# Kernel tuning notes

Measured on AMD Instinct MI355X. Metric: run time of the kernel, lower is better.

The kernel has to match this reference:

```python
import jax, jax.numpy as jnp
import numpy as np

N, E = 25000, 400000
D_NODE, D_EDGE_IN, D_EH, D_H, D_DUAL = 128, 16, 128, 256, 128


def layer_norm(x, g, b, eps=1e-5):
    mu = jnp.mean(x, axis=-1, keepdims=True)
    var = jnp.mean((x - mu) ** 2, axis=-1, keepdims=True)
    return (x - mu) * jax.lax.rsqrt(var + eps) * g + b


def setup_inputs() -> dict:
    key = jax.random.key(0)
    ks = jax.random.split(key, 20)

    def w(k, shape):
        return (jax.random.normal(k, shape, dtype=jnp.float32) * 0.05)

    inp = {
        "node_embedding": jax.random.normal(ks[0], (N, D_NODE), dtype=jnp.float32),
        "edge_index": jax.random.randint(ks[1], (2, E), 0, N, dtype=jnp.int64),
        "edge_attr": jax.random.normal(ks[2], (E, D_EDGE_IN), dtype=jnp.float32),
        "dual_node_emb": jax.random.normal(ks[3], (E, D_DUAL), dtype=jnp.float32),
        "atom_reactivity_logits": jax.random.normal(ks[4], (N,), dtype=jnp.float32),
        "W_be1": w(ks[5], (D_EDGE_IN, D_EH)), "b_be1": jnp.zeros((D_EH,), jnp.float32),
        "g_be1": jnp.ones((D_EH,), jnp.float32), "bb_be1": jnp.zeros((D_EH,), jnp.float32),
        "W_be2": w(ks[6], (D_EH, D_EH)), "b_be2": jnp.zeros((D_EH,), jnp.float32),
        "g_be2": jnp.ones((D_EH,), jnp.float32), "bb_be2": jnp.zeros((D_EH,), jnp.float32),
        "W_be3": w(ks[7], (D_EH, D_EH)), "b_be3": jnp.zeros((D_EH,), jnp.float32),
        "g_be3": jnp.ones((D_EH,), jnp.float32), "bb_be3": jnp.zeros((D_EH,), jnp.float32),
        # DualGraphBondReactivityPredictor
        "W_d1": w(ks[8], (D_DUAL, D_H)), "b_d1": jnp.zeros((D_H,), jnp.float32),
        "W_d2": w(ks[9], (D_H, D_H)), "b_d2": jnp.zeros((D_H,), jnp.float32),
        "W_do": w(ks[10], (D_H, 1)), "b_do": jnp.zeros((1,), jnp.float32),
        # main head: in = 2*D_NODE + D_EH + 3 = 387
        "W_f1": w(ks[11], (2 * D_NODE + D_EH + 3, D_H)), "b_f1": jnp.zeros((D_H,), jnp.float32),
        "W_f2": w(ks[12], (D_H, D_H)), "b_f2": jnp.zeros((D_H,), jnp.float32),
        "W_bo": w(ks[13], (D_H, 1)), "b_bo": jnp.zeros((1,), jnp.float32),
    }
    return inp


def reference(node_embedding, edge_index, edge_attr, dual_node_emb, atom_reactivity_logits,
              W_be1, b_be1, g_be1, bb_be1, W_be2, b_be2, g_be2, bb_be2,
              W_be3, b_be3, g_be3, bb_be3,
              W_d1, b_d1, W_d2, b_d2, W_do, b_do,
              W_f1, b_f1, W_f2, b_f2, W_bo, b_bo):
    src, dst = edge_index[0], edge_index[1]

    # BondEmbedding (dropout = identity in eval mode)
    e = jax.nn.silu(layer_norm(edge_attr @ W_be1 + b_be1, g_be1, bb_be1))
    e = jax.nn.silu(layer_norm(e @ W_be2 + b_be2, g_be2, bb_be2))
    e = jax.nn.silu(layer_norm(e @ W_be3 + b_be3, g_be3, bb_be3))  # [E, D_EH]

    atom_p = jax.nn.sigmoid(atom_reactivity_logits)  # [N]
    p_src = atom_p[src][:, None]  # [E,1]
    p_dst = atom_p[dst][:, None]

    # dual-graph bond reactivity
    d = jax.nn.silu(dual_node_emb @ W_d1 + b_d1)
    d = jax.nn.silu(d @ W_d2 + b_d2)
    dual_p = jax.nn.sigmoid((d @ W_do + b_do)[:, 0])[:, None]  # [E,1]

    feats = jnp.concatenate(
        [node_embedding[src], node_embedding[dst], e, dual_p, p_src, p_dst], axis=-1
    )  # [E, 2*D_NODE + D_EH + 3]

    x = jax.nn.silu(feats @ W_f1 + b_f1)
    x = jax.nn.silu(x @ W_f2 + b_f2)
    return (x @ W_bo + b_bo)[:, 0]  # [E]
```

## Files before the change

### kernel.cpp

```cpp
#include <hip/hip_runtime.h>
#include <hip/hip_bf16.h>
#include <stdint.h>

typedef __attribute__((ext_vector_type(8))) short bf16x8;
typedef __attribute__((ext_vector_type(4))) float f32x4;
typedef __attribute__((ext_vector_type(4))) float float4v;

__device__ __forceinline__ uint16_t bfc(float x){
    __hip_bfloat16 h = __float2bfloat16(x);
    return __builtin_bit_cast(uint16_t, h);
}
__device__ __forceinline__ uint32_t pk2(float a, float b){
    return (uint32_t)bfc(a) | ((uint32_t)bfc(b) << 16);
}
__device__ __forceinline__ float fsigmoid(float x){ return 1.0f / (1.0f + __expf(-x)); }
__device__ __forceinline__ float fsilu(float x){ return x * fsigmoid(x); }

__device__ __forceinline__ bf16x8 pack8(float4v lo, float4v hi){
    bf16x8 r;
    r[0]=(short)bfc(lo[0]); r[1]=(short)bfc(lo[1]);
    r[2]=(short)bfc(lo[2]); r[3]=(short)bfc(lo[3]);
    r[4]=(short)bfc(hi[0]); r[5]=(short)bfc(hi[1]);
    r[6]=(short)bfc(hi[2]); r[7]=(short)bfc(hi[3]);
    return r;
}

#define SZ_BE1 4096
#define SZ_128 16384
#define SZ_D1  32768
#define SZ_D2  65536
#define SZ_F1  98304
#define OFF_BE1 0
#define OFF_BE2 (OFF_BE1 + SZ_BE1)
#define OFF_BE3 (OFF_BE2 + SZ_128)
#define OFF_D1  (OFF_BE3 + SZ_128)
#define OFF_D2  (OFF_D1 + SZ_D1)
#define OFF_F1  (OFF_D2 + SZ_D2)
#define OFF_F2  (OFF_F1 + SZ_F1)
#define WS_ELEMS (OFF_F2 + SZ_D2)

__device__ __forceinline__ int fragpos(int k, int c, int OUT){
    int kt = k >> 5, ct = c >> 4;
    int fid = kt * (OUT >> 4) + ct;
    int ln = ((k & 31) >> 3) * 16 + (c & 15);
    return fid * 512 + ln * 8 + (k & 7);
}

__global__ void __launch_bounds__(256)
prep_w(const float* __restrict__ Wbe1, const float* __restrict__ Wbe2,
       const float* __restrict__ Wbe3, const float* __restrict__ Wd1,
       const float* __restrict__ Wd2,  const float* __restrict__ Wf1,
       const float* __restrict__ Wf2,  uint16_t* __restrict__ ws){
    int t = blockIdx.x * 256 + threadIdx.x;
    if (t >= WS_ELEMS) return;
    if (t < OFF_BE2) {
        int u = t;            int k = u >> 7, c = u & 127;
        float v = (k < 16) ? Wbe1[k * 128 + c] : 0.0f;
        ws[OFF_BE1 + fragpos(k, c, 128)] = bfc(v);
    } else if (t < OFF_BE3) {
        int u = t - OFF_BE2;  int k = u >> 7, c = u & 127;
        ws[OFF_BE2 + fragpos(k, c, 128)] = bfc(Wbe2[u]);
    } else if (t < OFF_D1) {
        int u = t - OFF_BE3;  int k = u >> 7, c = u & 127;
        ws[OFF_BE3 + fragpos(k, c, 128)] = bfc(Wbe3[u]);
    } else if (t < OFF_D2) {
        int u = t - OFF_D1;   int k = u >> 8, c = u & 255;
        ws[OFF_D1 + fragpos(k, c, 256)] = bfc(Wd1[u]);
    } else if (t < OFF_F1) {
        int u = t - OFF_D2;   int k = u >> 8, c = u & 255;
        ws[OFF_D2 + fragpos(k, c, 256)] = bfc(Wd2[u]);
    } else if (t < OFF_F2) {
        int u = t - OFF_F1;   int k = u >> 8, c = u & 255;
        ws[OFF_F1 + fragpos(k, c, 256)] = bfc(Wf1[u]);
    } else {
        int u = t - OFF_F2;   int k = u >> 8, c = u & 255;
        ws[OFF_F2 + fragpos(k, c, 256)] = bfc(Wf2[u]);
    }
}

__global__ void __launch_bounds__(256)
prep_n(const float* __restrict__ src, uint16_t* __restrict__ dst, int n){
    int t = blockIdx.x * 256 + threadIdx.x;
    if (t < n) dst[t] = bfc(src[t]);
}

typedef const __attribute__((address_space(1))) void gas_void;
typedef __attribute__((address_space(3))) void las_void;
__device__ __forceinline__ void g2l16(const void* g, void* l){
    __builtin_amdgcn_global_load_lds((gas_void*)g, (las_void*)l, 16, 0, 0);
}


__global__ void __launch_bounds__(512)
k_be(const float* __restrict__ edge_attr,
     const float* __restrict__ b_be1, const float* __restrict__ g_be1, const float* __restrict__ bb_be1,
     const float* __restrict__ b_be2, const float* __restrict__ g_be2, const float* __restrict__ bb_be2,
     const float* __restrict__ b_be3, const float* __restrict__ g_be3, const float* __restrict__ bb_be3,
     const uint16_t* __restrict__ ws, uint16_t* __restrict__ e3buf, int E)
{
    __shared__ char lds[49152];
    const int t = threadIdx.x, wave = t >> 6, lane = t & 63;
    const int li = lane & 15, lg = lane >> 4;
    const int e0b = blockIdx.x * 128;
    char* bufE = lds;
    uint16_t* wb0 = (uint16_t*)(lds + 32768);
    uint16_t* wb1 = (uint16_t*)(lds + 40960);
    const uint8_t* wsb = (const uint8_t*)ws;

    int cur = 0;
// ... 55 lines not shown
            const float* pa = edge_attr + (size_t)ea * 16 + lg * 8;
            aE = pack8(*(const float4v*)pa, *(const float4v*)(pa + 4));
        }
        grpBE(aE);
        lnstoreBE(g_be1, bb_be1);
        stepend();
    }
    initBE(b_be2);
    #pragma unroll 1
    for (int kt = 0; kt < 4; ++kt){
        stage8(kt < 3 ? OFF_BE2 + (kt + 1) * 4096 : OFF_BE3);
        grpBE(eb_read(wave * 16 + li, kt));
        if (kt == 3) lnstoreBE(g_be2, bb_be2);
        stepend();
    }
    initBE(b_be3);
    #pragma unroll 1
    for (int kt = 0; kt < 4; ++kt){
        if (kt < 3) stage8(OFF_BE3 + (kt + 1) * 4096);
        grpBE(eb_read(wave * 16 + li, kt));
        if (kt == 3) lnstoreBE(g_be3, bb_be3);
        stepend();
    }
    #pragma unroll
    for (int i = 0; i < 4; ++i){
        int b = t * 16 + i * 8192;
        int row = b >> 8;
        uint4 v = *(const uint4*)(bufE + (b ^ ((row & 7) << 4)));
        *(uint4*)((uint8_t*)e3buf + (size_t)e0b * 256 + b) = v;
    }
}

__global__ void __launch_bounds__(512)
k_d1(const float* __restrict__ dual_emb, const float* __restrict__ b_d1,
     const uint16_t* __restrict__ ws, uint16_t* __restrict__ hbuf, int E)
{
    __shared__ char lds[32768];
    const int t = threadIdx.x, wave = t >> 6, lane = t & 63;
    const int li = lane & 15, lg = lane >> 4;
    const int eg = wave >> 1, ch = wave & 1;
    const int e0b = blockIdx.x * 128;
    uint16_t* wb0 = (uint16_t*)lds;
    uint16_t* wb1 = (uint16_t*)(lds + 16384);
    const uint8_t* wsb = (const uint8_t*)ws;

    int cur = 0;
    auto stage16 = [&](int elemoff){
        uint8_t* dst = (uint8_t*)(cur ? wb0 : wb1) + t * 16;
        const uint8_t* g = wsb + (size_t)elemoff * 2 + t * 16;
        g2l16(g, dst); g2l16(g + 8192, dst + 8192);
    };
    auto stepend = [&](){ __syncthreads(); cur ^= 1; };
    auto curb = [&]() -> const uint16_t* { return cur ? wb1 : wb0; };

    f32x4 acc[2][8];
    #pragma unroll
    for (int ct = 0; ct < 8; ++ct){
        float bv = b_d1[ch * 128 + ct * 16 + li];
        f32x4 iv = {bv, bv, bv, bv};
        acc[0][ct] = iv; acc[1][ct] = iv;
    }

    {
        const uint8_t* g = wsb + (size_t)OFF_D1 * 2 + t * 16;
        g2l16(g, (uint8_t*)wb0 + t * 16);
        g2l16(g + 8192, (uint8_t*)wb0 + t * 16 + 8192);
    }
    __syncthreads();

    #pragma unroll 1
    for (int kt = 0; kt < 4; ++kt){
        if (kt < 3) stage16(OFF_D1 + (kt + 1) * 8192);
        bf16x8 a0, a1;
        {
            int ea = e0b + eg * 32 + li;      if (ea >= E) ea = E - 1;
            int eb = e0b + eg * 32 + 16 + li; if (eb >= E) eb = E - 1;
            const float* pa = dual_emb + (size_t)ea * 128 + kt * 32 + lg * 8;
            const float* pb = dual_emb + (size_t)eb * 128 + kt * 32 + lg * 8;
            a0 = pack8(*(const float4v*)pa, *(const float4v*)(pa + 4));
            a1 = pack8(*(const float4v*)pb, *(const float4v*)(pb + 4));
        }
        #pragma unroll
        for (int ct = 0; ct < 8; ++ct){
            bf16x8 b = *(const bf16x8*)(curb() + (ch * 8 + ct) * 512 + lane * 8);
            acc[0][ct] = __builtin_amdgcn_mfma_f32_16x16x32_bf16(a0, b, acc[0][ct], 0, 0, 0);
            acc[1][ct] = __builtin_amdgcn_mfma_f32_16x16x32_bf16(a1, b, acc[1][ct], 0, 0, 0);
        }
        if (kt < 3) stepend();
    }
    #pragma unroll
    for (int rt = 0; rt < 2; ++rt)
        #pragma unroll
        for (int r = 0; r < 4; ++r){
            size_t row = (size_t)(e0b + eg * 32 + rt * 16 + lg * 4 + r);
            #pragma unroll
            for (int ct = 0; ct < 8; ++ct)
                hbuf[row * 256 + ch * 128 + ct * 16 + li] = bfc(fsilu(acc[rt][ct][r]));
        }
}

__global__ void __launch_bounds__(512)
k_d2(const float* __restrict__ b_d2, const float* __restrict__ W_do, const float* __restrict__ b_do,
     const uint16_t* __restrict__ ws, const uint16_t* __restrict__ hbuf,
     float* __restrict__ dpbuf, int E)
{
    __shared__ char lds[33792];
    const int t = threadIdx.x, wave = t >> 6, lane = t & 63;
    const int li = lane & 15, lg = lane >> 4;
    const int eg = wave >> 1, ch = wave & 1;
    const int e0b = blockIdx.x * 128;
    uint16_t* wb0 = (uint16_t*)lds;
    uint16_t* wb1 = (uint16_t*)(lds + 16384);
    float* dpp = (float*)(lds + 32768);
    const uint8_t* wsb = (const uint8_t*)ws;

    int cur = 0;
    auto stage16 = [&](int elemoff){
        uint8_t* dst = (uint8_t*)(cur ? wb0 : wb1) + t * 16;
        const uint8_t* g = wsb + (size_t)elemoff * 2 + t * 16;
        g2l16(g, dst); g2l16(g + 8192, dst + 8192);
    };
    auto stepend = [&](){ __syncthreads(); cur ^= 1; };
    auto curb = [&]() -> const uint16_t* { return cur ? wb1 : wb0; };

    f32x4 acc[2][8];
    #pragma unroll
    for (int ct = 0; ct < 8; ++ct){
        float bv = b_d2[ch * 128 + ct * 16 + li];
        f32x4 iv = {bv, bv, bv, bv};
        acc[0][ct] = iv; acc[1][ct] = iv;
    }
    {
        const uint8_t* g = wsb + (size_t)OFF_D2 * 2 + t * 16;
        g2l16(g, (uint8_t*)wb0 + t * 16);
        g2l16(g + 8192, (uint8_t*)wb0 + t * 16 + 8192);
    }
    __syncthreads();

    #pragma unroll 1
    for (int kt = 0; kt < 8; ++kt){
        if (kt < 7) stage16(OFF_D2 + (kt + 1) * 8192);
        bf16x8 a0 = *(const bf16x8*)(hbuf + (size_t)(e0b + eg * 32 + li) * 256 + kt * 32 + lg * 8);
        bf16x8 a1 = *(const bf16x8*)(hbuf + (size_t)(e0b + eg * 32 + 16 + li) * 256 + kt * 32 + lg * 8);
        #pragma unroll
        for (int ct = 0; ct < 8; ++ct){
            bf16x8 b = *(const bf16x8*)(curb() + (ch * 8 + ct) * 512 + lane * 8);
            acc[0][ct] = __builtin_amdgcn_mfma_f32_16x16x32_bf16(a0, b, acc[0][ct], 0, 0, 0);
            acc[1][ct] = __builtin_amdgcn_mfma_f32_16x16x32_bf16(a1, b, acc[1][ct], 0, 0, 0);
        }
        if (kt < 7) stepend();
    }
    #pragma unroll
    for (int rt = 0; rt < 2; ++rt)
        #pragma unroll
        for (int r = 0; r < 4; ++r){
            float s = 0.f;
            #pragma unroll
            for (int ct = 0; ct < 8; ++ct)
                s += fsilu(acc[rt][ct][r]) * W_do[ch * 128 + ct * 16 + li];
            s += __shfl_xor(s, 1); s += __shfl_xor(s, 2);
            s += __shfl_xor(s, 4); s += __shfl_xor(s, 8);
            if (li == 0) dpp[ch * 128 + eg * 32 + rt * 16 + lg * 4 + r] = s;
        }
    __syncthreads();
    if (t < 128) dpbuf[e0b + t] = fsigmoid(dpp[t] + dpp[128 + t] + b_do[0]);
}

__global__ void __launch_bounds__(512)
k_f1(const int* __restrict__ edge_index, const float* __restrict__ logits,
     const float* __restrict__ W_f1, const float* __restrict__ b_f1,
     const uint16_t* __restrict__ ws, const uint16_t* __restrict__ nbf,
     const uint16_t* __restrict__ e3buf, const float* __restrict__ dpbuf,
     uint16_t* __restrict__ hbuf, int E)
{
    __shared__ char lds[34816];
    const int t = threadIdx.x, wave = t >> 6, lane = t & 63;
    const int li = lane & 15, lg = lane >> 4;
    const int eg = wave >> 1, ch = wave & 1;
    const int e0b = blockIdx.x * 128;
    uint16_t* wb0 = (uint16_t*)lds;
    uint16_t* wb1 = (uint16_t*)(lds + 16384);
    float* ps = (float*)(lds + 32768);
    float* pd = (float*)(lds + 33280);
    int* sidx = (int*)(lds + 33792);
    int* didx = (int*)(lds + 34304);
    const uint8_t* wsb = (const uint8_t*)ws;

    if (t < 128) {
        int e = e0b + t; if (e >= E) e = E - 1;
        int s_ = edge_index[e];
        int d_ = edge_index[E + e];
        sidx[t] = s_; didx[t] = d_;
        ps[t] = fsigmoid(logits[s_]);
        pd[t] = fsigmoid(logits[d_]);
    }
    int cur = 0;
    auto stage16 = [&](int elemoff){
        uint8_t* dst = (uint8_t*)(cur ? wb0 : wb1) + t * 16;
        const uint8_t* g = wsb + (size_t)elemoff * 2 + t * 16;
        g2l16(g, dst); g2l16(g + 8192, dst + 8192);
    };
    auto stepend = [&](){ __syncthreads(); cur ^= 1; };
    auto curb = [&]() -> const uint16_t* { return cur ? wb1 : wb0; };

    {
        const uint8_t* g = wsb + (size_t)OFF_F1 * 2 + t * 16;
        g2l16(g, (uint8_t*)wb0 + t * 16);
        g2l16(g + 8192, (uint8_t*)wb0 + t * 16 + 8192);
    }
    __syncthreads();

    f32x4 acc[2][8];
    {
        #pragma unroll
        for (int ct = 0; ct < 8; ++ct){
            int col = ch * 128 + ct * 16 + li;
            float bv = b_f1[col];
            float t0 = W_f1[384 * 256 + col];
            float t1 = W_f1[385 * 256 + col];
            float t2 = W_f1[386 * 256 + col];
            #pragma unroll
            for (int rt = 0; rt < 2; ++rt)
                #pragma unroll
                for (int r = 0; r < 4; ++r){
                    int row = eg * 32 + rt * 16 + lg * 4 + r;
                    float dv = dpbuf[e0b + row];
                    acc[rt][ct][r] = bv + dv*t0 + ps[row]*t1 + pd[row]*t2;
                }
        }
    }
    int s0 = sidx[eg * 32 + li],  s1 = sidx[eg * 32 + 16 + li];
    int d0 = didx[eg * 32 + li],  d1 = didx[eg * 32 + 16 + li];
    #pragma unroll 1
    for (int kt = 0; kt < 12; ++kt){
        if (kt < 11) stage16(OFF_F1 + (kt + 1) * 8192);
        bf16x8 a0, a1;
        if (kt < 8){
            int ra = (kt < 4) ? s0 : d0;
            int rb = (kt < 4) ? s1 : d1;
            int ko = (kt & 3) * 32 + lg * 8;
            a0 = *(const bf16x8*)(nbf + (size_t)ra * 128 + ko);
            a1 = *(const bf16x8*)(nbf + (size_t)rb * 128 + ko);
        } else {
            int ko = (kt - 8) * 32 + lg * 8;
            a0 = *(const bf16x8*)(e3buf + (size_t)(e0b + eg * 32 + li) * 128 + ko);
            a1 = *(const bf16x8*)(e3buf + (size_t)(e0b + eg * 32 + 16 + li) * 128 + ko);
        }
        #pragma unroll
        for (int ct = 0; ct < 8; ++ct){
            bf16x8 b = *(const bf16x8*)(curb() + (ch * 8 + ct) * 512 + lane * 8);
            acc[0][ct] = __builtin_amdgcn_mfma_f32_16x16x32_bf16(a0, b, acc[0][ct], 0, 0, 0);
            acc[1][ct] = __builtin_amdgcn_mfma_f32_16x16x32_bf16(a1, b, acc[1][ct], 0, 0, 0);
        }
        if (kt < 11) stepend();
    }
    #pragma unroll
    for (int rt = 0; rt < 2; ++rt)
        #pragma unroll
        for (int r = 0; r < 4; ++r){
            size_t row = (size_t)(e0b + eg * 32 + rt * 16 + lg * 4 + r);
            #pragma unroll
            for (int ct = 0; ct < 8; ++ct)
                hbuf[row * 256 + ch * 128 + ct * 16 + li] = bfc(fsilu(acc[rt][ct][r]));
        }
}

__global__ void __launch_bounds__(512)
k_f2(const float* __restrict__ b_f2, const float* __restrict__ W_bo, const float* __restrict__ b_bo,
     const uint16_t* __restrict__ ws, const uint16_t* __restrict__ hbuf,
     float* __restrict__ out, int E)
{
    __shared__ char lds[33792];
    const int t = threadIdx.x, wave = t >> 6, lane = t & 63;
    const int li = lane & 15, lg = lane >> 4;
    const int eg = wave >> 1, ch = wave & 1;
    const int e0b = blockIdx.x * 128;
    uint16_t* wb0 = (uint16_t*)lds;
    uint16_t* wb1 = (uint16_t*)(lds + 16384);
    float* bop = (float*)(lds + 32768);
    const uint8_t* wsb = (const uint8_t*)ws;

    int cur = 0;
    auto stage16 = [&](int elemoff){
        uint8_t* dst = (uint8_t*)(cur ? wb0 : wb1) + t * 16;
        const uint8_t* g = wsb + (size_t)elemoff * 2 + t * 16;
        g2l16(g, dst); g2l16(g + 8192, dst + 8192);
    };
    auto stepend = [&](){ __syncthreads(); cur ^= 1; };
    auto curb = [&]() -> const uint16_t* { return cur ? wb1 : wb0; };

    f32x4 acc[2][8];
    #pragma unroll
    for (int ct = 0; ct < 8; ++ct){
        float bv = b_f2[ch * 128 + ct * 16 + li];
        f32x4 iv = {bv, bv, bv, bv};
        acc[0][ct] = iv; acc[1][ct] = iv;
    }
    {
        const uint8_t* g = wsb + (size_t)OFF_F2 * 2 + t * 16;
        g2l16(g, (uint8_t*)wb0 + t * 16);
        g2l16(g + 8192, (uint8_t*)wb0 + t * 16 + 8192);
    }
    __syncthreads();

    #pragma unroll 1
    for (int kt = 0; kt < 8; ++kt){
        if (kt < 7) stage16(OFF_F2 + (kt + 1) * 8192);
        bf16x8 a0 = *(const bf16x8*)(hbuf + (size_t)(e0b + eg * 32 + li) * 256 + kt * 32 + lg * 8);
        bf16x8 a1 = *(const bf16x8*)(hbuf + (size_t)(e0b + eg * 32 + 16 + li) * 256 + kt * 32 + lg * 8);
        #pragma unroll
        for (int ct = 0; ct < 8; ++ct){
            bf16x8 b = *(const bf16x8*)(curb() + (ch * 8 + ct) * 512 + lane * 8);
            acc[0][ct] = __builtin_amdgcn_mfma_f32_16x16x32_bf16(a0, b, acc[0][ct], 0, 0, 0);
            acc[1][ct] = __builtin_amdgcn_mfma_f32_16x16x32_bf16(a1, b, acc[1][ct], 0, 0, 0);
        }
        if (kt < 7) stepend();
    }
    #pragma unroll
    for (int rt = 0; rt < 2; ++rt)
        #pragma unroll
        for (int r = 0; r < 4; ++r){
            float s = 0.f;
            #pragma unroll
            for (int ct = 0; ct < 8; ++ct)
                s += fsilu(acc[rt][ct][r]) * W_bo[ch * 128 + ct * 16 + li];
            s += __shfl_xor(s, 1); s += __shfl_xor(s, 2);
            s += __shfl_xor(s, 4); s += __shfl_xor(s, 8);
            if (li == 0) bop[ch * 128 + eg * 32 + rt * 16 + lg * 4 + r] = s;
        }
    __syncthreads();
    if (t < 128){
        int e = e0b + t;
        if (e < E) out[e] = bop[t] + bop[128 + t] + b_bo[0];
    }
}

#define LDS_TOTAL 135168
__global__ void __launch_bounds__(512) __attribute__((amdgpu_waves_per_eu(2, 2)))
bond_fast_kernel(const int* __restrict__ edge_index,
                 const float* __restrict__ edge_attr, const float* __restrict__ dual_emb,
                 const float* __restrict__ logits,
                 const float* __restrict__ b_be1, const float* __restrict__ g_be1, const float* __restrict__ bb_be1,
                 const float* __restrict__ b_be2, const float* __restrict__ g_be2, const float* __restrict__ bb_be2,
                 const float* __restrict__ b_be3, const float* __restrict__ g_be3, const float* __restrict__ bb_be3,
                 const float* __restrict__ b_d1, const float* __restrict__ b_d2,
                 const float* __restrict__ W_do, const float* __restrict__ b_do,
                 const float* __restrict__ W_f1, const float* __restrict__ b_f1,
                 const float* __restrict__ b_f2,
                 const float* __restrict__ W_bo, const float* __restrict__ b_bo,
                 const uint16_t* __restrict__ ws, float* __restrict__ out, int E)
{
    __shared__ char lds[LDS_TOTAL];
    const int t    = threadIdx.x;
    const int wave = t >> 6;
    const int lane = t & 63;
    const int li   = lane & 15, lg = lane >> 4;
    const int eg   = wave >> 1;
    const int ch   = wave & 1;
    const int e0b  = blockIdx.x * 128;

    char* bufE = lds;
    char* h256 = lds + 32768;
    uint16_t* wb0 = (uint16_t*)(lds + 98304);
    uint16_t* wb1 = (uint16_t*)(lds + 114688);
    float* ps  = (float*)(lds + 131072);
    float* pd  = (float*)(lds + 131584);
// ... 9 lines not shown
        int e = e0b + t; if (e >= E) e = E - 1;
        int s_ = edge_index[e];
        int d_ = edge_index[E + e];
        sidx[t] = s_; didx[t] = d_;
        ps[t] = fsigmoid(logits[s_]);
        pd[t] = fsigmoid(logits[d_]);
    }

    int cur = 0;
    auto stageW = [&](int elemoff, int big){
        uint8_t* dst = (uint8_t*)(cur ? wb0 : wb1) + t * 16;
        const uint8_t* g = wsb + (size_t)elemoff * 2 + t * 16;
        g2l16(g, dst);
        if (big) g2l16(g + 8192, dst + 8192);
    };
    auto stepend = [&](){ __syncthreads(); cur ^= 1; };
    auto curbuf  = [&]() -> const uint16_t* { return cur ? wb1 : wb0; };

    f32x4 acc[2][8];

    auto ldf = [&](const uint16_t* w, int fid) -> bf16x8 {
        return *(const bf16x8*)(w + fid * 512 + lane * 8);
    };
    auto grpBE = [&](const uint16_t* w, bf16x8 a0){
        #pragma unroll
        for (int ct = 0; ct < 8; ++ct){
            bf16x8 b = ldf(w, ct);
            acc[0][ct] = __builtin_amdgcn_mfma_f32_16x16x32_bf16(a0, b, acc[0][ct], 0, 0, 0);
        }
    };
    auto grp256 = [&](const uint16_t* w, bf16x8 a0, bf16x8 a1){
        #pragma unroll
        for (int ct = 0; ct < 8; ++ct){
            bf16x8 b = ldf(w, ch * 8 + ct);
            acc[0][ct] = __builtin_amdgcn_mfma_f32_16x16x32_bf16(a0, b, acc[0][ct], 0, 0, 0);
            acc[1][ct] = __builtin_amdgcn_mfma_f32_16x16x32_bf16(a1, b, acc[1][ct], 0, 0, 0);
        }
    };
    auto initBE = [&](const float* b){
        #pragma unroll
        for (int ct = 0; ct < 8; ++ct){
            float bv = b[li + 16 * ct];
            f32x4 iv = {bv, bv, bv, bv};
            acc[0][ct] = iv;
        }
    };
    auto init256 = [&](const float* b){
        #pragma unroll
        for (int ct = 0; ct < 8; ++ct){
            float bv = b[ch * 128 + ct * 16 + li];
            f32x4 iv = {bv, bv, bv, bv};
            acc[0][ct] = iv; acc[1][ct] = iv;
        }
    };
    auto eb_read = [&](int row, int kt) -> bf16x8 {
        int off = row * 256 + (kt * 32 + lg * 8) * 2;
        return *(const bf16x8*)(bufE + (off ^ ((row & 7) << 4)));
    };
    auto h2_read = [&](int row, int kt) -> bf16x8 {
        int off = row * 512 + (kt * 32 + lg * 8) * 2;
        return *(const bf16x8*)(h256 + (off ^ ((row & 7) << 4)));
    };
    auto lnstoreBE = [&](const float* g, const float* bb){
        #pragma unroll
        for (int r = 0; r < 4; ++r){
            float s = 0.f, q = 0.f;
            #pragma unroll
// ... 513 lines not shown
                              hipStream_t stream) {
    const float* node_emb   = (const float*)d_in[0];
    const int*   edge_index = (const int*)d_in[1];
    const float* edge_attr  = (const float*)d_in[2];
    const float* dual_emb   = (const float*)d_in[3];
    const float* logits     = (const float*)d_in[4];
    const float* W_be1 = (const float*)d_in[5];
    const float* b_be1 = (const float*)d_in[6];
    const float* g_be1 = (const float*)d_in[7];
    const float* bb_be1= (const float*)d_in[8];
    const float* W_be2 = (const float*)d_in[9];
    const float* b_be2 = (const float*)d_in[10];
    const float* g_be2 = (const float*)d_in[11];
    const float* bb_be2= (const float*)d_in[12];
    const float* W_be3 = (const float*)d_in[13];
    const float* b_be3 = (const float*)d_in[14];
    const float* g_be3 = (const float*)d_in[15];
    const float* bb_be3= (const float*)d_in[16];
    const float* W_d1  = (const float*)d_in[17];
    const float* b_d1  = (const float*)d_in[18];
    const float* W_d2  = (const float*)d_in[19];
    const float* b_d2  = (const float*)d_in[20];
    const float* W_do  = (const float*)d_in[21];
    const float* b_do  = (const float*)d_in[22];
    const float* W_f1  = (const float*)d_in[23];
    const float* b_f1  = (const float*)d_in[24];
    const float* W_f2  = (const float*)d_in[25];
    const float* b_f2  = (const float*)d_in[26];
    const float* W_bo  = (const float*)d_in[27];
    const float* b_bo  = (const float*)d_in[28];
    float* out = (float*)d_out;

    int E = in_sizes[2] / 16;
    int nblocks = (E + 127) / 128;
    size_t Epad = (size_t)nblocks * 128;
    size_t nodeElems = (size_t)in_sizes[0];
    size_t wsNeedSmall = ((size_t)WS_ELEMS + nodeElems) * 2;
    size_t wsNeedBig = ((size_t)WS_ELEMS + nodeElems + Epad * 128 + Epad * 256) * 2 + Epad * 4;

    if (ws_size >= wsNeedBig) {
        uint16_t* ws16  = (uint16_t*)d_ws;
        uint16_t* nbf_g = ws16 + WS_ELEMS;
        uint16_t* e3buf = nbf_g + nodeElems;
        uint16_t* hbuf  = e3buf + Epad * 128;
        float*    dpbuf = (float*)(hbuf + Epad * 256);
        prep_w<<<dim3((WS_ELEMS + 255) / 256), dim3(256), 0, stream>>>(
            W_be1, W_be2, W_be3, W_d1, W_d2, W_f1, W_f2, ws16);
        prep_n<<<dim3((int)((nodeElems + 255) / 256)), dim3(256), 0, stream>>>(
            node_emb, nbf_g, (int)nodeElems);
        k_be<<<dim3(nblocks), dim3(512), 0, stream>>>(
            edge_attr, b_be1, g_be1, bb_be1, b_be2, g_be2, bb_be2,
            b_be3, g_be3, bb_be3, ws16, e3buf, E);
        k_d1<<<dim3(nblocks), dim3(512), 0, stream>>>(dual_emb, b_d1, ws16, hbuf, E);
        k_d2<<<dim3(nblocks), dim3(512), 0, stream>>>(b_d2, W_do, b_do, ws16, hbuf, dpbuf, E);
        k_f1<<<dim3(nblocks), dim3(512), 0, stream>>>(
            edge_index, logits, W_f1, b_f1, ws16, nbf_g, e3buf, dpbuf, hbuf, E);
        k_f2<<<dim3(nblocks), dim3(512), 0, stream>>>(b_f2, W_bo, b_bo, ws16, hbuf, out, E);
    } else if (ws_size >= wsNeedSmall) {
        uint16_t* ws16 = (uint16_t*)d_ws;
        prep_w<<<dim3((WS_ELEMS + 255) / 256), dim3(256), 0, stream>>>(
            W_be1, W_be2, W_be3, W_d1, W_d2, W_f1, W_f2, ws16);
        prep_n<<<dim3((int)((nodeElems + 255) / 256)), dim3(256), 0, stream>>>(
            node_emb, ws16 + WS_ELEMS, (int)nodeElems);
        bond_fast_kernel<<<dim3(nblocks), dim3(512), 0, stream>>>(
            edge_index, edge_attr, dual_emb, logits,
            b_be1, g_be1, bb_be1,
            b_be2, g_be2, bb_be2,
            b_be3, g_be3, bb_be3,
            b_d1, b_d2, W_do, b_do,
            W_f1, b_f1, b_f2, W_bo, b_bo,
            ws16, out, E);
    } else {
        bond_fused_kernel<<<dim3(nblocks), dim3(512), 0, stream>>>(
            node_emb, edge_index, edge_attr, dual_emb, logits,
            W_be1, b_be1, g_be1, bb_be1,
            W_be2, b_be2, g_be2, bb_be2,
            W_be3, b_be3, g_be3, bb_be3,
            W_d1, b_d1, W_d2, b_d2, W_do, b_do,
            W_f1, b_f1, W_f2, b_f2, W_bo, b_bo,
            out, E);
    }
}
```

Measured before the change: 691.4 us.

## Fuse dual and final MLP layer pairs into single kernels keeping hidden in LDS

Merges k_d1/k_d2 and k_f1/k_f2 into two kernels that keep the 256-wide hidden activation in swizzled LDS instead of round-tripping it through a global bf16 buffer. Blocks shrink to 64 edges and the weight layout is permuted so each half-step stages 8KB of fragments with finer-grained double buffering. This removes about 200MB of hidden-buffer traffic and two launches. In exchange there are twice as many barriers per K step, more LDS per block (possibly lower occupancy), and less weight reuse per staged tile.

Measured after the change: 706.1 us. +2.1%, slower.

```diff
diff --git a/kernel.cpp b/kernel.cpp
--- a/kernel.cpp
+++ b/kernel.cpp
@@ -39,9 +39,15 @@
 #define OFF_F2  (OFF_F1 + SZ_F1)
 #define WS_ELEMS (OFF_F2 + SZ_D2)
 
-__device__ __forceinline__ int fragpos(int k, int c, int OUT){
-    int kt = k >> 5, ct = c >> 4;
-    int fid = kt * (OUT >> 4) + ct;
+__device__ __forceinline__ int fragpos128(int k, int c){
+    int fid = (k >> 5) * 8 + (c >> 4);
+    int ln = ((k & 31) >> 3) * 16 + (c & 15);
+    return fid * 512 + ln * 8 + (k & 7);
+}
+__device__ __forceinline__ int fragpos256(int k, int c){
+    int ct = c >> 4;
+    int pos = (ct & 3) + ((ct >> 2) & 1) * 8 + ((ct >> 3) & 1) * 4;
+    int fid = (k >> 5) * 16 + pos;
     int ln = ((k & 31) >> 3) * 16 + (c & 15);
     return fid * 512 + ln * 8 + (k & 7);
 }
@@ -56,25 +62,25 @@
     if (t < OFF_BE2) {
         int u = t;            int k = u >> 7, c = u & 127;
         float v = (k < 16) ? Wbe1[k * 128 + c] : 0.0f;
-        ws[OFF_BE1 + fragpos(k, c, 128)] = bfc(v);
+        ws[OFF_BE1 + fragpos128(k, c)] = bfc(v);
     } else if (t < OFF_BE3) {
         int u = t - OFF_BE2;  int k = u >> 7, c = u & 127;
-        ws[OFF_BE2 + fragpos(k, c, 128)] = bfc(Wbe2[u]);
+        ws[OFF_BE2 + fragpos128(k, c)] = bfc(Wbe2[u]);
     } else if (t < OFF_D1) {
         int u = t - OFF_BE3;  int k = u >> 7, c = u & 127;
-        ws[OFF_BE3 + fragpos(k, c, 128)] = bfc(Wbe3[u]);
+        ws[OFF_BE3 + fragpos128(k, c)] = bfc(Wbe3[u]);
     } else if (t < OFF_D2) {
         int u = t - OFF_D1;   int k = u >> 8, c = u & 255;
-        ws[OFF_D1 + fragpos(k, c, 256)] = bfc(Wd1[u]);
+        ws[OFF_D1 + fragpos256(k, c)] = bfc(Wd1[u]);
     } else if (t < OFF_F1) {
         int u = t - OFF_D2;   int k = u >> 8, c = u & 255;
-        ws[OFF_D2 + fragpos(k, c, 256)] = bfc(Wd2[u]);
+        ws[OFF_D2 + fragpos256(k, c)] = bfc(Wd2[u]);
     } else if (t < OFF_F2) {
         int u = t - OFF_F1;   int k = u >> 8, c = u & 255;
-        ws[OFF_F1 + fragpos(k, c, 256)] = bfc(Wf1[u]);
+        ws[OFF_F1 + fragpos256(k, c)] = bfc(Wf1[u]);
     } else {
         int u = t - OFF_F2;   int k = u >> 8, c = u & 255;
-        ws[OFF_F2 + fragpos(k, c, 256)] = bfc(Wf2[u]);
+        ws[OFF_F2 + fragpos256(k, c)] = bfc(Wf2[u]);
     }
 }
 
@@ -196,161 +202,145 @@
 }
 
 __global__ void __launch_bounds__(512)
-k_d1(const float* __restrict__ dual_emb, const float* __restrict__ b_d1,
-     const uint16_t* __restrict__ ws, uint16_t* __restrict__ hbuf, int E)
+k_d12(const float* __restrict__ dual_emb,
+      const float* __restrict__ b_d1, const float* __restrict__ b_d2,
+      const float* __restrict__ W_do, const float* __restrict__ b_do,
+      const uint16_t* __restrict__ ws, float* __restrict__ dpbuf, int E)
 {
-    __shared__ char lds[32768];
+    __shared__ char lds[50176];
     const int t = threadIdx.x, wave = t >> 6, lane = t & 63;
     const int li = lane & 15, lg = lane >> 4;
     const int eg = wave >> 1, ch = wave & 1;
-    const int e0b = blockIdx.x * 128;
-    uint16_t* wb0 = (uint16_t*)lds;
-    uint16_t* wb1 = (uint16_t*)(lds + 16384);
+    const int e0b = blockIdx.x * 64;
+    char* h256 = lds;
+    uint16_t* wb0 = (uint16_t*)(lds + 32768);
+    uint16_t* wb1 = (uint16_t*)(lds + 40960);
+    float* dpp = (float*)(lds + 49152);
+    float* dpv = (float*)(lds + 49664);
     const uint8_t* wsb = (const uint8_t*)ws;
 
     int cur = 0;
-    auto stage16 = [&](int elemoff){
-        uint8_t* dst = (uint8_t*)(cur ? wb0 : wb1) + t * 16;
-        const uint8_t* g = wsb + (size_t)elemoff * 2 + t * 16;
-        g2l16(g, dst); g2l16(g + 8192, dst + 8192);
+    auto stage8 = [&](int elemoff){
+        g2l16(wsb + (size_t)elemoff * 2 + t * 16, (uint8_t*)(cur ? wb0 : wb1) + t * 16);
     };
     auto stepend = [&](){ __syncthreads(); cur ^= 1; };
     auto curb = [&]() -> const uint16_t* { return cur ? wb1 : wb0; };
 
-    f32x4 acc[2][8];
-    #pragma unroll
-    for (int ct = 0; ct < 8; ++ct){
-        float bv = b_d1[ch * 128 + ct * 16 + li];
-        f32x4 iv = {bv, bv, bv, bv};
-        acc[0][ct] = iv; acc[1][ct] = iv;
-    }
-
-    {
-        const uint8_t* g = wsb + (size_t)OFF_D1 * 2 + t * 16;
-        g2l16(g, (uint8_t*)wb0 + t * 16);
-        g2l16(g + 8192, (uint8_t*)wb0 + t * 16 + 8192);
-    }
+    f32x4 acc[8];
+    auto ldf = [&](int fid) -> bf16x8 { return *(const bf16x8*)(curb() + fid * 512 + lane * 8); };
+    auto h2_read = [&](int row, int kt) -> bf16x8 {
+        int off = row * 512 + (kt * 32 + lg * 8) * 2;
+        return *(const bf16x8*)(h256 + (off ^ ((row & 7) << 4)));
+    };
+    auto init256 = [&](const float* b){
+        #pragma unroll
+        for (int j = 0; j < 8; ++j){
+            float bv = b[ch * 128 + j * 16 + li];
+            f32x4 iv = {bv, bv, bv, bv};
+            acc[j] = iv;
+        }
+    };
+    auto mfma4lo = [&](bf16x8 a){
+        acc[0] = __builtin_amdgcn_mfma_f32_16x16x32_bf16(a, ldf(ch*4+0), acc[0], 0, 0, 0);
+        acc[1] = __builtin_amdgcn_mfma_f32_16x16x32_bf16(a, ldf(ch*4+1), acc[1], 0, 0, 0);
+        acc[2] = __builtin_amdgcn_mfma_f32_16x16x32_bf16(a, ldf(ch*4+2), acc[2], 0, 0, 0);
+        acc[3] = __builtin_amdgcn_mfma_f32_16x16x32_bf16(a, ldf(ch*4+3), acc[3], 0, 0, 0);
+    };
+    auto mfma4hi = [&](bf16x8 a){
+        acc[4] = __builtin_amdgcn_mfma_f32_16x16x32_bf16(a, ldf(ch*4+0), acc[4], 0, 0, 0);
+        acc[5] = __builtin_amdgcn_mfma_f32_16x16x32_bf16(a, ldf(ch*4+1), acc[5], 0, 0, 0);
+        acc[6] = __builtin_amdgcn_mfma_f32_16x16x32_bf16(a, ldf(ch*4+2), acc[6], 0, 0, 0);
+        acc[7] = __builtin_amdgcn_mfma_f32_16x16x32_bf16(a, ldf(ch*4+3), acc[7], 0, 0, 0);
+    };
+    auto silustore256 = [&](){
+        #pragma unroll
+        for (int r = 0; r < 4; ++r){
+            int row = eg * 16 + lg * 4 + r;
+            int rswz = (row & 7) << 4;
+            #pragma unroll
+            for (int j = 0; j < 8; ++j){
+                int off = row * 512 + (ch * 128 + j * 16 + li) * 2;
+                *(uint16_t*)(h256 + (off ^ rswz)) = bfc(fsilu(acc[j][r]));
+            }
+        }
+    };
+
+    g2l16(wsb + (size_t)OFF_D1 * 2 + t * 16, (uint8_t*)wb0 + t * 16);
     __syncthreads();
 
+    init256(b_d1);
     #pragma unroll 1
     for (int kt = 0; kt < 4; ++kt){
-        if (kt < 3) stage16(OFF_D1 + (kt + 1) * 8192);
-        bf16x8 a0, a1;
+        stage8(OFF_D1 + (2 * kt + 1) * 4096);
+        bf16x8 aD;
         {
-            int ea = e0b + eg * 32 + li;      if (ea >= E) ea = E - 1;
-            int eb = e0b + eg * 32 + 16 + li; if (eb >= E) eb = E - 1;
+            int ea = e0b + eg * 16 + li; if (ea >= E) ea = E - 1;
             const float* pa = dual_emb + (size_t)ea * 128 + kt * 32 + lg * 8;
-            const float* pb = dual_emb + (size_t)eb * 128 + kt * 32 + lg * 8;
-            a0 = pack8(*(const float4v*)pa, *(const float4v*)(pa + 4));
-            a1 = pack8(*(const float4v*)pb, *(const float4v*)(pb + 4));
-        }
-        #pragma unroll
-        for (int ct = 0; ct < 8; ++ct){
-            bf16x8 b = *(const bf16x8*)(curb() + (ch * 8 + ct) * 512 + lane * 8);
-            acc[0][ct] = __builtin_amdgcn_mfma_f32_16x16x32_bf16(a0, b, acc[0][ct], 0, 0, 0);
-            acc[1][ct] = __builtin_amdgcn_mfma_f32_16x16x32_bf16(a1, b, acc[1][ct], 0, 0, 0);
-        }
-        if (kt < 3) stepend();
-    }
-    #pragma unroll
-    for (int rt = 0; rt < 2; ++rt)
-        #pragma unroll
-        for (int r = 0; r < 4; ++r){
-            size_t row = (size_t)(e0b + eg * 32 + rt * 16 + lg * 4 + r);
-            #pragma unroll
-            for (int ct = 0; ct < 8; ++ct)
-                hbuf[row * 256 + ch * 128 + ct * 16 + li] = bfc(fsilu(acc[rt][ct][r]));
-        }
+            aD = pack8(*(const float4v*)pa, *(const float4v*)(pa + 4));
+        }
+        mfma4lo(aD);
+        stepend();
+        stage8(kt < 3 ? OFF_D1 + (2 * kt + 2) * 4096 : OFF_D2);
+        mfma4hi(aD);
+        if (kt == 3) silustore256();
+        stepend();
+    }
+
+    init256(b_d2);
+    #pragma unroll 1
+    for (int kt = 0; kt < 8; ++kt){
+        stage8(OFF_D2 + (2 * kt + 1) * 4096);
+        bf16x8 aD = h2_read(eg * 16 + li, kt);
+        mfma4lo(aD);
+        stepend();
+        if (kt < 7) stage8(OFF_D2 + (2 * kt + 2) * 4096);
+        mfma4hi(aD);
+        if (kt == 7){
+            #pragma unroll
+            for (int r = 0; r < 4; ++r){
+                float s = 0.f;
+                #pragma unroll
+                for (int j = 0; j < 8; ++j)
+                    s += fsilu(acc[j][r]) * W_do[ch * 128 + j * 16 + li];
+                s += __shfl_xor(s, 1); s += __shfl_xor(s, 2);
+                s += __shfl_xor(s, 4); s += __shfl_xor(s, 8);
+                if (li == 0) dpp[ch * 64 + eg * 16 + lg * 4 + r] = s;
+            }
+        }
+        stepend();
+    }
+    if (t < 64){
+        int e = e0b + t;
+        if (e < E) dpbuf[e] = fsigmoid(dpp[t] + dpp[64 + t] + b_do[0]);
+        else       dpbuf[e] = 0.f;
+    }
 }
 
 __global__ void __launch_bounds__(512)
-k_d2(const float* __restrict__ b_d2, const float* __restrict__ W_do, const float* __restrict__ b_do,
-     const uint16_t* __restrict__ ws, const uint16_t* __restrict__ hbuf,
-     float* __restrict__ dpbuf, int E)
+k_f12(const int* __restrict__ edge_index, const float* __restrict__ logits,
+      const float* __restrict__ W_f1, const float* __restrict__ b_f1,
+      const float* __restrict__ b_f2,
+      const float* __restrict__ W_bo, const float* __restrict__ b_bo,
+      const uint16_t* __restrict__ ws, const uint16_t* __restrict__ nbf,
+      const uint16_t* __restrict__ e3buf, const float* __restrict__ dpbuf,
+      float* __restrict__ out, int E)
 {
-    __shared__ char lds[33792];
+    __shared__ char lds[50688];
     const int t = threadIdx.x, wave = t >> 6, lane = t & 63;
     const int li = lane & 15, lg = lane >> 4;
     const int eg = wave >> 1, ch = wave & 1;
-    const int e0b = blockIdx.x * 128;
-    uint16_t* wb0 = (uint16_t*)lds;
-    uint16_t* wb1 = (uint16_t*)(lds + 16384);
-    float* dpp = (float*)(lds + 32768);
+    const int e0b = blockIdx.x * 64;
+    char* h256 = lds;
+    uint16_t* wb0 = (uint16_t*)(lds + 32768);
+    uint16_t* wb1 = (uint16_t*)(lds + 40960);
+    float* ps = (float*)(lds + 49152);
+    float* pd = (float*)(lds + 49408);
+    int* sidx = (int*)(lds + 49664);
+    int* didx = (int*)(lds + 49920);
+    float* bop = (float*)(lds + 50176);
     const uint8_t* wsb = (const uint8_t*)ws;
 
-    int cur = 0;
-    auto stage16 = [&](int elemoff){
-        uint8_t* dst = (uint8_t*)(cur ? wb0 : wb1) + t * 16;
-        const uint8_t* g = wsb + (size_t)elemoff * 2 + t * 16;
-        g2l16(g, dst); g2l16(g + 8192, dst + 8192);
-    };
-    auto stepend = [&](){ __syncthreads(); cur ^= 1; };
-    auto curb = [&]() -> const uint16_t* { return cur ? wb1 : wb0; };
-
-    f32x4 acc[2][8];
-    #pragma unroll
-    for (int ct = 0; ct < 8; ++ct){
-        float bv = b_d2[ch * 128 + ct * 16 + li];
-        f32x4 iv = {bv, bv, bv, bv};
-        acc[0][ct] = iv; acc[1][ct] = iv;
-    }
-    {
-        const uint8_t* g = wsb + (size_t)OFF_D2 * 2 + t * 16;
-        g2l16(g, (uint8_t*)wb0 + t * 16);
-        g2l16(g + 8192, (uint8_t*)wb0 + t * 16 + 8192);
-    }
-    __syncthreads();
-
-    #pragma unroll 1
-    for (int kt = 0; kt < 8; ++kt){
-        if (kt < 7) stage16(OFF_D2 + (kt + 1) * 8192);
-        bf16x8 a0 = *(const bf16x8*)(hbuf + (size_t)(e0b + eg * 32 + li) * 256 + kt * 32 + lg * 8);
-        bf16x8 a1 = *(const bf16x8*)(hbuf + (size_t)(e0b + eg * 32 + 16 + li) * 256 + kt * 32 + lg * 8);
-        #pragma unroll
-        for (int ct = 0; ct < 8; ++ct){
-            bf16x8 b = *(const bf16x8*)(curb() + (ch * 8 + ct) * 512 + lane * 8);
-            acc[0][ct] = __builtin_amdgcn_mfma_f32_16x16x32_bf16(a0, b, acc[0][ct], 0, 0, 0);
-            acc[1][ct] = __builtin_amdgcn_mfma_f32_16x16x32_bf16(a1, b, acc[1][ct], 0, 0, 0);
-        }
-        if (kt < 7) stepend();
-    }
-    #pragma unroll
-    for (int rt = 0; rt < 2; ++rt)
-        #pragma unroll
-        for (int r = 0; r < 4; ++r){
-            float s = 0.f;
-            #pragma unroll
-            for (int ct = 0; ct < 8; ++ct)
-                s += fsilu(acc[rt][ct][r]) * W_do[ch * 128 + ct * 16 + li];
-            s += __shfl_xor(s, 1); s += __shfl_xor(s, 2);
-            s += __shfl_xor(s, 4); s += __shfl_xor(s, 8);
-            if (li == 0) dpp[ch * 128 + eg * 32 + rt * 16 + lg * 4 + r] = s;
-        }
-    __syncthreads();
-    if (t < 128) dpbuf[e0b + t] = fsigmoid(dpp[t] + dpp[128 + t] + b_do[0]);
-}
-
-__global__ void __launch_bounds__(512)
-k_f1(const int* __restrict__ edge_index, const float* __restrict__ logits,
-     const float* __restrict__ W_f1, const float* __restrict__ b_f1,
-     const uint16_t* __restrict__ ws, const uint16_t* __restrict__ nbf,
-     const uint16_t* __restrict__ e3buf, const float* __restrict__ dpbuf,
-     uint16_t* __restrict__ hbuf, int E)
-{
-    __shared__ char lds[34816];
-    const int t = threadIdx.x, wave = t >> 6, lane = t & 63;
-    const int li = lane & 15, lg = lane >> 4;
-    const int eg = wave >> 1, ch = wave & 1;
-    const int e0b = blockIdx.x * 128;
-    uint16_t* wb0 = (uint16_t*)lds;
-    uint16_t* wb1 = (uint16_t*)(lds + 16384);
-    float* ps = (float*)(lds + 32768);
-    float* pd = (float*)(lds + 33280);
-    int* sidx = (int*)(lds + 33792);
-    int* didx = (int*)(lds + 34304);
-    const uint8_t* wsb = (const uint8_t*)ws;
-
-    if (t < 128) {
+    if (t < 64) {
         int e = e0b + t; if (e >= E) e = E - 1;
         int s_ = edge_index[e];
         int d_ = edge_index[E + e];
@@ -359,143 +349,116 @@
         pd[t] = fsigmoid(logits[d_]);
     }
     int cur = 0;
-    auto stage16 = [&](int elemoff){
-        uint8_t* dst = (uint8_t*)(cur ? wb0 : wb1) + t * 16;
-        const uint8_t* g = wsb + (size_t)elemoff * 2 + t * 16;
-        g2l16(g, dst); g2l16(g + 8192, dst + 8192);
+    auto stage8 = [&](int elemoff){
+        g2l16(wsb + (size_t)elemoff * 2 + t * 16, (uint8_t*)(cur ? wb0 : wb1) + t * 16);
     };
     auto stepend = [&](){ __syncthreads(); cur ^= 1; };
     auto curb = [&]() -> const uint16_t* { return cur ? wb1 : wb0; };
 
+    f32x4 acc[8];
+    auto ldf = [&](int fid) -> bf16x8 { return *(const bf16x8*)(curb() + fid * 512 + lane * 8); };
+    auto h2_read = [&](int row, int kt) -> bf16x8 {
+        int off = row * 512 + (kt * 32 + lg * 8) * 2;
+        return *(const bf16x8*)(h256 + (off ^ ((row & 7) << 4)));
+    };
+    auto init256 = [&](const float* b){
+        #pragma unroll
+        for (int j = 0; j < 8; ++j){
+            float bv = b[ch * 128 + j * 16 + li];
+            f32x4 iv = {bv, bv, bv, bv};
+            acc[j] = iv;
+        }
+    };
+    auto mfma4lo = [&](bf16x8 a){
+        acc[0] = __builtin_amdgcn_mfma_f32_16x16x32_bf16(a, ldf(ch*4+0), acc[0], 0, 0, 0);
+        acc[1] = __builtin_amdgcn_mfma_f32_16x16x32_bf16(a, ldf(ch*4+1), acc[1], 0, 0, 0);
+        acc[2] = __builtin_amdgcn_mfma_f32_16x16x32_bf16(a, ldf(ch*4+2), acc[2], 0, 0, 0);
+        acc[3] = __builtin_amdgcn_mfma_f32_16x16x32_bf16(a, ldf(ch*4+3), acc[3], 0, 0, 0);
+    };
+    auto mfma4hi = [&](bf16x8 a){
+        acc[4] = __builtin_amdgcn_mfma_f32_16x16x32_bf16(a, ldf(ch*4+0), acc[4], 0, 0, 0);
+        acc[5] = __builtin_amdgcn_mfma_f32_16x16x32_bf16(a, ldf(ch*4+1), acc[5], 0, 0, 0);
+        acc[6] = __builtin_amdgcn_mfma_f32_16x16x32_bf16(a, ldf(ch*4+2), acc[6], 0, 0, 0);
+        acc[7] = __builtin_amdgcn_mfma_f32_16x16x32_bf16(a, ldf(ch*4+3), acc[7], 0, 0, 0);
+    };
+    auto silustore256 = [&](){
+        #pragma unroll
+        for (int r = 0; r < 4; ++r){
+            int row = eg * 16 + lg * 4 + r;
+            int rswz = (row & 7) << 4;
+            #pragma unroll
+            for (int j = 0; j < 8; ++j){
+                int off = row * 512 + (ch * 128 + j * 16 + li) * 2;
+                *(uint16_t*)(h256 + (off ^ rswz)) = bfc(fsilu(acc[j][r]));
+            }
+        }
+    };
+
+    g2l16(wsb + (size_t)OFF_F1 * 2 + t * 16, (uint8_t*)wb0 + t * 16);
+    __syncthreads();
+
     {
-        const uint8_t* g = wsb + (size_t)OFF_F1 * 2 + t * 16;
-        g2l16(g, (uint8_t*)wb0 + t * 16);
-        g2l16(g + 8192, (uint8_t*)wb0 + t * 16 + 8192);
-    }
-    __syncthreads();
-
-    f32x4 acc[2][8];
-    {
-        #pragma unroll
-        for (int ct = 0; ct < 8; ++ct){
-            int col = ch * 128 + ct * 16 + li;
+        float dvv[4], psr[4], pdr[4];
+        #pragma unroll
+        for (int r = 0; r < 4; ++r){
+            int row = eg * 16 + lg * 4 + r;
+            dvv[r] = dpbuf[e0b + row]; psr[r] = ps[row]; pdr[r] = pd[row];
+        }
+        #pragma unroll
+        for (int j = 0; j < 8; ++j){
+            int col = ch * 128 + j * 16 + li;
             float bv = b_f1[col];
             float t0 = W_f1[384 * 256 + col];
             float t1 = W_f1[385 * 256 + col];
             float t2 = W_f1[386 * 256 + col];
             #pragma unroll
-            for (int rt = 0; rt < 2; ++rt)
-                #pragma unroll
-                for (int r = 0; r < 4; ++r){
-                    int row = eg * 32 + rt * 16 + lg * 4 + r;
-                    float dv = dpbuf[e0b + row];
-                    acc[rt][ct][r] = bv + dv*t0 + ps[row]*t1 + pd[row]*t2;
-                }
-        }
-    }
-    int s0 = sidx[eg * 32 + li],  s1 = sidx[eg * 32 + 16 + li];
-    int d0 = didx[eg * 32 + li],  d1 = didx[eg * 32 + 16 + li];
+            for (int r = 0; r < 4; ++r)
+                acc[j][r] = bv + dvv[r]*t0 + psr[r]*t1 + pdr[r]*t2;
+        }
+    }
+    int sv = sidx[eg * 16 + li];
+    int dv = didx[eg * 16 + li];
     #pragma unroll 1
     for (int kt = 0; kt < 12; ++kt){
-        if (kt < 11) stage16(OFF_F1 + (kt + 1) * 8192);
-        bf16x8 a0, a1;
-        if (kt < 8){
-            int ra = (kt < 4) ? s0 : d0;
-            int rb = (kt < 4) ? s1 : d1;
-            int ko = (kt & 3) * 32 + lg * 8;
-            a0 = *(const bf16x8*)(nbf + (size_t)ra * 128 + ko);
-            a1 = *(const bf16x8*)(nbf + (size_t)rb * 128 + ko);
-        } else {
-            int ko = (kt - 8) * 32 + lg * 8;
-            a0 = *(const bf16x8*)(e3buf + (size_t)(e0b + eg * 32 + li) * 128 + ko);
-            a1 = *(const bf16x8*)(e3buf + (size_t)(e0b + eg * 32 + 16 + li) * 128 + ko);
-        }
-        #pragma unroll
-        for (int ct = 0; ct < 8; ++ct){
-            bf16x8 b = *(const bf16x8*)(curb() + (ch * 8 + ct) * 512 + lane * 8);
-            acc[0][ct] = __builtin_amdgcn_mfma_f32_16x16x32_bf16(a0, b, acc[0][ct], 0, 0, 0);
-            acc[1][ct] = __builtin_amdgcn_mfma_f32_16x16x32_bf16(a1, b, acc[1][ct], 0, 0, 0);
-        }
-        if (kt < 11) stepend();
-    }
-    #pragma unroll
-    for (int rt = 0; rt < 2; ++rt)
-        #pragma unroll
-        for (int r = 0; r < 4; ++r){
-            size_t row = (size_t)(e0b + eg * 32 + rt * 16 + lg * 4 + r);
-            #pragma unroll
-            for (int ct = 0; ct < 8; ++ct)
-                hbuf[row * 256 + ch * 128 + ct * 16 + li] = bfc(fsilu(acc[rt][ct][r]));
-        }
-}
-
-__global__ void __launch_bounds__(512)
-k_f2(const float* __restrict__ b_f2, const float* __restrict__ W_bo, const float* __restrict__ b_bo,
-     const uint16_t* __restrict__ ws, const uint16_t* __restrict__ hbuf,
-     float* __restrict__ out, int E)
-{
-    __shared__ char lds[33792];
-    const int t = threadIdx.x, wave = t >> 6, lane = t & 63;
-    const int li = lane & 15, lg = lane >> 4;
-    const int eg = wave >> 1, ch = wave & 1;
-    const int e0b = blockIdx.x * 128;
-    uint16_t* wb0 = (uint16_t*)lds;
-    uint16_t* wb1 = (uint16_t*)(lds + 16384);
-    float* bop = (float*)(lds + 32768);
-    const uint8_t* wsb = (const uint8_t*)ws;
-
-    int cur = 0;
-    auto stage16 = [&](int elemoff){
-        uint8_t* dst = (uint8_t*)(cur ? wb0 : wb1) + t * 16;
-        const uint8_t* g = wsb + (size_t)elemoff * 2 + t * 16;
-        g2l16(g, dst); g2l16(g + 8192, dst + 8192);
-    };
-    auto stepend = [&](){ __syncthreads(); cur ^= 1; };
-    auto curb = [&]() -> const uint16_t* { return cur ? wb1 : wb0; };
-
-    f32x4 acc[2][8];
-    #pragma unroll
-    for (int ct = 0; ct < 8; ++ct){
-        float bv = b_f2[ch * 128 + ct * 16 + li];
-        f32x4 iv = {bv, bv, bv, bv};
-        acc[0][ct] = iv; acc[1][ct] = iv;
-    }
-    {
-        const uint8_t* g = wsb + (size_t)OFF_F2 * 2 + t * 16;
-        g2l16(g, (uint8_t*)wb0 + t * 16);
-        g2l16(g + 8192, (uint8_t*)wb0 + t * 16 + 8192);
-    }
-    __syncthreads();
-
+        stage8(OFF_F1 + (2 * kt + 1) * 4096);
+        bf16x8 aD;
+        if (kt < 4)      aD = *(const bf16x8*)(nbf + (size_t)sv * 128 + kt * 32 + lg * 8);
+        else if (kt < 8) aD = *(const bf16x8*)(nbf + (size_t)dv * 128 + (kt - 4) * 32 + lg * 8);
+        else             aD = *(const bf16x8*)(e3buf + (size_t)(e0b + eg * 16 + li) * 128 + (kt - 8) * 32 + lg * 8);
+        mfma4lo(aD);
+        stepend();
+        stage8(kt < 11 ? OFF_F1 + (2 * kt + 2) * 4096 : OFF_F2);
+        mfma4hi(aD);
+        if (kt == 11) silustore256();
+        stepend();
+    }
+
+    init256(b_f2);
     #pragma unroll 1
     for (int kt = 0; kt < 8; ++kt){
-        if (kt < 7) stage16(OFF_F2 + (kt + 1) * 8192);
-        bf16x8 a0 = *(const bf16x8*)(hbuf + (size_t)(e0b + eg * 32 + li) * 256 + kt * 32 + lg * 8);
-        bf16x8 a1 = *(const bf16x8*)(hbuf + (size_t)(e0b + eg * 32 + 16 + li) * 256 + kt * 32 + lg * 8);
-        #pragma unroll
-        for (int ct = 0; ct < 8; ++ct){
-            bf16x8 b = *(const bf16x8*)(curb() + (ch * 8 + ct) * 512 + lane * 8);
-            acc[0][ct] = __builtin_amdgcn_mfma_f32_16x16x32_bf16(a0, b, acc[0][ct], 0, 0, 0);
-            acc[1][ct] = __builtin_amdgcn_mfma_f32_16x16x32_bf16(a1, b, acc[1][ct], 0, 0, 0);
-        }
-        if (kt < 7) stepend();
-    }
-    #pragma unroll
-    for (int rt = 0; rt < 2; ++rt)
-        #pragma unroll
-        for (int r = 0; r < 4; ++r){
-            float s = 0.f;
-            #pragma unroll
-            for (int ct = 0; ct < 8; ++ct)
-                s += fsilu(acc[rt][ct][r]) * W_bo[ch * 128 + ct * 16 + li];
-            s += __shfl_xor(s, 1); s += __shfl_xor(s, 2);
-            s += __shfl_xor(s, 4); s += __shfl_xor(s, 8);
-            if (li == 0) bop[ch * 128 + eg * 32 + rt * 16 + lg * 4 + r] = s;
-        }
-    __syncthreads();
-    if (t < 128){
+        stage8(OFF_F2 + (2 * kt + 1) * 4096);
+        bf16x8 aD = h2_read(eg * 16 + li, kt);
+        mfma4lo(aD);
+        stepend();
+        if (kt < 7) stage8(OFF_F2 + (2 * kt + 2) * 4096);
+        mfma4hi(aD);
+        if (kt == 7){
+            #pragma unroll
+            for (int r = 0; r < 4; ++r){
+                float s = 0.f;
+                #pragma unroll
+                for (int j = 0; j < 8; ++j)
+                    s += fsilu(acc[j][r]) * W_bo[ch * 128 + j * 16 + li];
+                s += __shfl_xor(s, 1); s += __shfl_xor(s, 2);
+                s += __shfl_xor(s, 4); s += __shfl_xor(s, 8);
+                if (li == 0) bop[ch * 64 + eg * 16 + lg * 4 + r] = s;
+            }
+        }
+        stepend();
+    }
+    if (t < 64){
         int e = e0b + t;
-        if (e < E) out[e] = bop[t] + bop[128 + t] + b_bo[0];
+        if (e < E) out[e] = bop[t] + bop[64 + t] + b_bo[0];
     }
 }
 
@@ -571,7 +534,8 @@
     auto grp256 = [&](const uint16_t* w, bf16x8 a0, bf16x8 a1){
         #pragma unroll
         for (int ct = 0; ct < 8; ++ct){
-            bf16x8 b = ldf(w, ch * 8 + ct);
+            int fid = (ct & 3) + ((ct >> 2) & 1) * 8 + ch * 4;
+            bf16x8 b = ldf(w, fid);
             acc[0][ct] = __builtin_amdgcn_mfma_f32_16x16x32_bf16(a0, b, acc[0][ct], 0, 0, 0);
             acc[1][ct] = __builtin_amdgcn_mfma_f32_16x16x32_bf16(a1, b, acc[1][ct], 0, 0, 0);
         }
@@ -1151,37 +1115,37 @@
     float* out = (float*)d_out;
 
     int E = in_sizes[2] / 16;
-    int nblocks = (E + 127) / 128;
-    size_t Epad = (size_t)nblocks * 128;
+    int nblocks128 = (E + 127) / 128;
+    int nblocks64  = (E + 63) / 64;
+    size_t Epad = (size_t)nblocks128 * 128;
     size_t nodeElems = (size_t)in_sizes[0];
     size_t wsNeedSmall = ((size_t)WS_ELEMS + nodeElems) * 2;
-    size_t wsNeedBig = ((size_t)WS_ELEMS + nodeElems + Epad * 128 + Epad * 256) * 2 + Epad * 4;
+    size_t wsNeedBig = ((size_t)WS_ELEMS + nodeElems + Epad * 128) * 2 + Epad * 4;
 
     if (ws_size >= wsNeedBig) {
         uint16_t* ws16  = (uint16_t*)d_ws;
         uint16_t* nbf_g = ws16 + WS_ELEMS;
         uint16_t* e3buf = nbf_g + nodeElems;
-        uint16_t* hbuf  = e3buf + Epad * 128;
-        float*    dpbuf = (float*)(hbuf + Epad * 256);
+        float*    dpbuf = (float*)(e3buf + Epad * 128);
         prep_w<<<dim3((WS_ELEMS + 255) / 256), dim3(256), 0, stream>>>(
             W_be1, W_be2, W_be3, W_d1, W_d2, W_f1, W_f2, ws16);
         prep_n<<<dim3((int)((nodeElems + 255) / 256)), dim3(256), 0, stream>>>(
             node_emb, nbf_g, (int)nodeElems);
-        k_be<<<dim3(nblocks), dim3(512), 0, stream>>>(
+        k_be<<<dim3(nblocks128), dim3(512), 0, stream>>>(
             edge_attr, b_be1, g_be1, bb_be1, b_be2, g_be2, bb_be2,
             b_be3, g_be3, bb_be3, ws16, e3buf, E);
-        k_d1<<<dim3(nblocks), dim3(512), 0, stream>>>(dual_emb, b_d1, ws16, hbuf, E);
-        k_d2<<<dim3(nblocks), dim3(512), 0, stream>>>(b_d2, W_do, b_do, ws16, hbuf, dpbuf, E);
-        k_f1<<<dim3(nblocks), dim3(512), 0, stream>>>(
-            edge_index, logits, W_f1, b_f1, ws16, nbf_g, e3buf, dpbuf, hbuf, E);
-        k_f2<<<dim3(nblocks), dim3(512), 0, stream>>>(b_f2, W_bo, b_bo, ws16, hbuf, out, E);
+        k_d12<<<dim3(nblocks64), dim3(512), 0, stream>>>(
+            dual_emb, b_d1, b_d2, W_do, b_do, ws16, dpbuf, E);
+        k_f12<<<dim3(nblocks64), dim3(512), 0, stream>>>(
+            edge_index, logits, W_f1, b_f1, b_f2, W_bo, b_bo,
+            ws16, nbf_g, e3buf, dpbuf, out, E);
     } else if (ws_size >= wsNeedSmall) {
         uint16_t* ws16 = (uint16_t*)d_ws;
         prep_w<<<dim3((WS_ELEMS + 255) / 256), dim3(256), 0, stream>>>(
             W_be1, W_be2, W_be3, W_d1, W_d2, W_f1, W_f2, ws16);
         prep_n<<<dim3((int)((nodeElems + 255) / 256)), dim3(256), 0, stream>>>(
             node_emb, ws16 + WS_ELEMS, (int)nodeElems);
-        bond_fast_kernel<<<dim3(nblocks), dim3(512), 0, stream>>>(
+        bond_fast_kernel<<<dim3(nblocks128), dim3(512), 0, stream>>>(
             edge_index, edge_attr, dual_emb, logits,
             b_be1, g_be1, bb_be1,
             b_be2, g_be2, bb_be2,
@@ -1190,7 +1154,7 @@
             W_f1, b_f1, b_f2, W_bo, b_bo,
             ws16, out, E);
     } else {
-        bond_fused_kernel<<<dim3(nblocks), dim3(512), 0, stream>>>(
+        bond_fused_kernel<<<dim3(nblocks128), dim3(512), 0, stream>>>(
             node_emb, edge_index, edge_attr, dual_emb, logits,
             W_be1, b_be1, g_be1, bb_be1,
             W_be2, b_be2, g_be2, bb_be2,
```
